# Performance work log

Measured on AMD Instinct MI355X. Metric: run time of the kernel, lower is better.

## Reference

```python
import jax, jax.numpy as jnp
import numpy as np

EPS = 1e-5
N0 = 2000  # number of crystals


def batchnorm(x, gamma, beta):
    # training-mode BatchNorm1d over rows (biased variance, like torch normalization)
    mu = jnp.mean(x, axis=0)
    var = jnp.mean(jnp.square(x - mu), axis=0)
    return (x - mu) * jax.lax.rsqrt(var + EPS) * gamma + beta


def setup_inputs() -> dict:
    key = jax.random.key(0)
    ks = jax.random.split(key, 16)
    N, M, F, B = 100000, 12, 64, 41
    d = {
        "atom_fea": jax.random.normal(ks[0], (N, 92), jnp.float32),
        "nbr_fea": jax.random.uniform(ks[1], (N, M, B), jnp.float32),
        "nbr_fea_idx": jax.random.randint(ks[2], (N, M), 0, N),
        "crystal_atom_idx": jnp.sort(jax.random.randint(ks[3], (N,), 0, N0)),
        "emb_w": jax.random.normal(ks[4], (92, F), jnp.float32) * 0.1,
        "emb_b": jax.random.normal(ks[5], (F,), jnp.float32) * 0.1,
        "conv_w": jax.random.normal(ks[6], (3, 2 * F + B, 2 * F), jnp.float32) * 0.05,
        "conv_b": jax.random.normal(ks[7], (3, 2 * F), jnp.float32) * 0.05,
        "bn1_g": jnp.ones((3, 2 * F), jnp.float32),
        "bn1_b": jnp.zeros((3, 2 * F), jnp.float32),
        "bn2_g": jnp.ones((3, F), jnp.float32),
        "bn2_b": jnp.zeros((3, F), jnp.float32),
        "fc_w": jax.random.normal(ks[8], (F, 128), jnp.float32) * 0.1,
        "fc_b": jax.random.normal(ks[9], (128,), jnp.float32) * 0.1,
        "head_w": jax.random.normal(ks[10], (128, 256), jnp.float32) * 0.1,
        "head_b": jax.random.normal(ks[11], (256,), jnp.float32) * 0.1,
        "out_w": jax.random.normal(ks[12], (256, 1), jnp.float32) * 0.1,
        "out_b": jax.random.normal(ks[13], (1,), jnp.float32) * 0.1,
    }
    return d


def reference(atom_fea, nbr_fea, nbr_fea_idx, crystal_atom_idx,
              emb_w, emb_b, conv_w, conv_b, bn1_g, bn1_b, bn2_g, bn2_b,
              fc_w, fc_b, head_w, head_b, out_w, out_b):
    N, M = nbr_fea_idx.shape
    F = emb_w.shape[1]
    x = atom_fea @ emb_w + emb_b  # (N, F)
    for i in range(conv_w.shape[0]):
        nbr_atom = x[nbr_fea_idx]  # (N, M, F) gather
        self_fea = jnp.broadcast_to(x[:, None, :], (N, M, F))
        tot = jnp.concatenate([self_fea, nbr_atom, nbr_fea], axis=2)  # (N, M, 2F+B)
        g = jnp.einsum('nmc,cf->nmf', tot, conv_w[i]) + conv_b[i]  # (N, M, 2F)
        g = batchnorm(g.reshape(N * M, 2 * F), bn1_g[i], bn1_b[i]).reshape(N, M, 2 * F)
        nbr_filter = jax.nn.sigmoid(g[:, :, :F])
        nbr_core = jax.nn.softplus(g[:, :, F:])
        nbr_sumed = jnp.sum(nbr_filter * nbr_core, axis=1)  # (N, F)
        nbr_sumed = batchnorm(nbr_sumed, bn2_g[i], bn2_b[i])
        x = jax.nn.softplus(x + nbr_sumed)
    # mean-pool atoms into crystals
    seg = crystal_atom_idx
    sums = jax.ops.segment_sum(x, seg, num_segments=N0)
    cnts = jax.ops.segment_sum(jnp.ones((N,), x.dtype), seg, num_segments=N0)
    crys = sums / jnp.maximum(cnts, 1.0)[:, None]  # (N0, F)
    crys = jax.nn.relu(crys @ fc_w + fc_b)
    h = crys @ head_w + head_b
    out = h @ out_w + out_b
    return out
```

## Files before the change

kernel.cpp:

```cpp
#include <hip/hip_runtime.h>
#include <hip/hip_bf16.h>

#define NATOM 100000
#define MNBR  12
#define FDIM  64
#define BDIM  41
#define C2    128
#define EPSBN 1e-5f
#define NEDGE (NATOM * MNBR)
#define KP48  48
#define NFRAG  16384
#define NFRAGS 8192

typedef __attribute__((ext_vector_type(8))) short bf16x8;
typedef __attribute__((ext_vector_type(4))) unsigned short u16x4;
typedef __attribute__((ext_vector_type(4))) float f32x4;

#define X_OFF    0L
#define XB_OFF   6400000L
#define S_OFF    9600000L
#define NBRB_OFF 16000000L
#define AS_OFF   54400000L
#define BALL_OFF 60800000L
#define BALLS_OFF 60808192L
#define BN1S_OFF 60812288L
#define BN2S_OFF 60828672L
#define SC1_OFF  60836864L
#define SH1_OFF  60836992L
#define SC2_OFF  60837120L
#define SH2_OFF  60837184L
#define CRY_OFF  60837248L
#define CNT_OFF  60965248L
#define ZB_OFF   60967296L
#define WS_NEED_FUSED ((ZB_OFF + 76800000L) * 4L)
#define ZERO_OFF BN1S_OFF
#define ZERO_CNT 154960L

__device__ __forceinline__ float bf2f(unsigned short u) {
    return __uint_as_float(((unsigned)u) << 16);
}
__device__ __forceinline__ unsigned short f2bf(float f) {
    __hip_bfloat16 h = __float2bfloat16(f);
    return *(unsigned short*)&h;
}
__device__ __forceinline__ float softplus_f(float v) {
    return fmaxf(v, 0.f) + __logf(1.f + __expf(-fabsf(v)));
}

__global__ void k_zero(float* __restrict__ p, long cnt) {
    long i = (long)blockIdx.x * 256 + threadIdx.x;
    if (i < cnt) p[i] = 0.f;
}

__global__ void k_nbrcvt(const float* __restrict__ nbr, __hip_bfloat16* __restrict__ outb) {
    long i = (long)blockIdx.x * 256 + threadIdx.x;
    if (i >= (long)NEDGE * 6) return;
    long e = i / 6;
    int c = (int)(i - e * 6);
    const float* src = nbr + e * BDIM + c * 8;
    bf16x8 v;
#pragma unroll
    for (int j = 0; j < 8; ++j) {
        int k = c * 8 + j;
        float f = (k < BDIM) ? src[j] : 0.f;
        v[j] = (short)f2bf(f);
    }
    *(bf16x8*)((short*)outb + e * KP48 + c * 8) = v;
}

__global__ void k_bcvt(const float* __restrict__ cw, __hip_bfloat16* __restrict__ ballf,
                       __hip_bfloat16* __restrict__ ballfS) {
    int i = blockIdx.x * 256 + threadIdx.x;
    if (i < NFRAG) {
        int T = i / 2048, r = i - T * 2048;
        int lidx = (r >> 3) & 63, e = i & 7;
        int s4 = r >> 9;
        int lo = lidx & 15, hi = lidx >> 4;
        int krow = 64 + s4 * 32 + hi * 8 + e;
        float v = (krow < 169) ? cw[krow * C2 + T * 16 + lo] : 0.f;
        ballf[i] = __float2bfloat16(v);
    } else if (i < NFRAG + NFRAGS) {
        int i2 = i - NFRAG;
        int T = i2 / 1024, r = i2 - T * 1024;
        int lidx = (r >> 3) & 63, e = i2 & 7;
        int s = r >> 9;
        int lo = lidx & 15, hi = lidx >> 4;
        int krow = s * 32 + hi * 8 + e;
        ballfS[i2] = __float2bfloat16(cw[krow * C2 + T * 16 + lo]);
    }
}

__global__ __launch_bounds__(256)
void k_embed(const float* __restrict__ af, const float* __restrict__ ew,
             const float* __restrict__ eb, float* __restrict__ x,
             __hip_bfloat16* __restrict__ xb) {
    int t = threadIdx.x;
    int c = t & 63, ag = t >> 6;
    long n0 = (long)blockIdx.x * 16 + ag * 4;
    float acc[4] = {0.f, 0.f, 0.f, 0.f};
    for (int k4 = 0; k4 < 23; ++k4) {
        float w0 = ew[(4 * k4 + 0) * FDIM + c];
        float w1 = ew[(4 * k4 + 1) * FDIM + c];
        float w2 = ew[(4 * k4 + 2) * FDIM + c];
        float w3 = ew[(4 * k4 + 3) * FDIM + c];
#pragma unroll
        for (int a = 0; a < 4; ++a) {
            const float4* ar = (const float4*)(af + (n0 + a) * 92);
            float4 v = ar[k4];
            acc[a] += v.x * w0 + v.y * w1 + v.z * w2 + v.w * w3;
        }
    }
    float b = eb[c];
#pragma unroll
    for (int a = 0; a < 4; ++a) {
        float v = acc[a] + b;
        x[(n0 + a) * FDIM + c] = v;
        xb[(n0 + a) * FDIM + c] = __float2bfloat16(v);
    }
}

__global__ __launch_bounds__(256, 8)
void k_lin(const __hip_bfloat16* __restrict__ xb, const __hip_bfloat16* __restrict__ ballfS,
           __hip_bfloat16* __restrict__ aS) {
    int t = threadIdx.x, w = t >> 6, l = t & 63;
    int lo = l & 15, hi = l >> 4;
    long atom0 = ((long)blockIdx.x * 4 + w) * 16;
    if (atom0 >= NATOM) return;
    const short* xs = (const short*)xb + (atom0 + lo) * FDIM + hi * 8;
    bf16x8 A0 = *(const bf16x8*)(xs);
    bf16x8 A1 = *(const bf16x8*)(xs + 32);
    const short* bS = (const short*)ballfS;
#pragma unroll
    for (int T = 0; T < 8; ++T) {
        bf16x8 B0 = *(const bf16x8*)(bS + T * 1024 + l * 8);
        bf16x8 B1 = *(const bf16x8*)(bS + T * 1024 + 512 + l * 8);
        f32x4 z = {0.f, 0.f, 0.f, 0.f};
        z = __builtin_amdgcn_mfma_f32_16x16x32_bf16(A0, B0, z, 0, 0, 0);
        z = __builtin_amdgcn_mfma_f32_16x16x32_bf16(A1, B1, z, 0, 0, 0);
#pragma unroll
        for (int qq = 0; qq < 4; ++qq)
            aS[(atom0 + hi * 4 + qq) * C2 + T * 16 + lo] = __float2bfloat16(z[qq]);
    }
}

template <int APPLY, int ZSTORE>
__global__ __launch_bounds__(256, 4)
void k_edge(const __hip_bfloat16* __restrict__ xb,
            const __hip_bfloat16* __restrict__ nbrb,
            const __hip_bfloat16* __restrict__ ballf,
            const __hip_bfloat16* __restrict__ aS,
            const int* __restrict__ idxp,
            const float* __restrict__ sc1, const float* __restrict__ sh1,
            float* __restrict__ bn1_slots,
            float* __restrict__ sout, float* __restrict__ bn2_slots,
            __hip_bfloat16* __restrict__ zb) {
    __shared__ float bn_s[256];
    __shared__ float sc_s[128], sh_s[128];

    const int t = threadIdx.x;
    const int w = t >> 6, l = t & 63;
    const int lo = l & 15, hi = l >> 4;
    const bool real = lo < MNBR;
    const int elo = real ? lo : 0;
    const int atom0 = blockIdx.x * 16 + w * 4;
    const short* xbS = (const short*)xb;
    const short* nbS = (const short*)nbrb;
    const short* aSS = (const short*)aS;
    const short* bb  = (const short*)ballf;
    short* zbS = (short*)zb;

    bn_s[t] = 0.f;
    if (APPLY && t < 128) { sc_s[t] = sc1[t]; sh_s[t] = sh1[t]; }
    __syncthreads();

    const bf16x8 zz = {0, 0, 0, 0, 0, 0, 0, 0};
    const int off1 = (hi < 2) ? (32 + hi * 8) : 0;

#pragma unroll 1
    for (int pr = 0; pr < 2; ++pr) {
        const int a0 = atom0 + pr * 2;
        const int a1 = a0 + 1;
        const int j0 = idxp[(long)a0 * MNBR + elo];
        const int j1 = idxp[(long)a1 * MNBR + elo];
        const short* xj0 = xbS + (long)j0 * FDIM + hi * 8;
        const short* xj1 = xbS + (long)j1 * FDIM + hi * 8;
        const short* nb0 = nbS + ((long)a0 * MNBR + elo) * KP48;
        const short* nb1 = nbS + ((long)a1 * MNBR + elo) * KP48;
        bf16x8 A00 = *(const bf16x8*)(xj0);
        bf16x8 A01 = *(const bf16x8*)(xj0 + 32);
        bf16x8 A02 = *(const bf16x8*)(nb0 + hi * 8);
        bf16x8 n03 = *(const bf16x8*)(nb0 + off1);
        bf16x8 A03 = (hi < 2) ? n03 : zz;
        bf16x8 A10 = *(const bf16x8*)(xj1);
        bf16x8 A11 = *(const bf16x8*)(xj1 + 32);
        bf16x8 A12 = *(const bf16x8*)(nb1 + hi * 8);
        bf16x8 n13 = *(const bf16x8*)(nb1 + off1);
        bf16x8 A13 = (hi < 2) ? n13 : zz;

        if (APPLY == 0) {
#pragma unroll 2
            for (int P = 0; P < 8; ++P) {
                const short* bp = bb + P * 2048 + l * 8;
                bf16x8 B0 = *(const bf16x8*)(bp);
                bf16x8 B1 = *(const bf16x8*)(bp + 512);
                bf16x8 B2 = *(const bf16x8*)(bp + 1024);
                bf16x8 B3 = *(const bf16x8*)(bp + 1536);
                float a0v = bf2f((unsigned short)aSS[(long)a0 * C2 + P * 16 + lo]);
                float a1v = bf2f((unsigned short)aSS[(long)a1 * C2 + P * 16 + lo]);
                f32x4 z0 = {0.f, 0.f, 0.f, 0.f}, z1 = {0.f, 0.f, 0.f, 0.f};
                z0 = __builtin_amdgcn_mfma_f32_16x16x32_bf16(A00, B0, z0, 0, 0, 0);
                z1 = __builtin_amdgcn_mfma_f32_16x16x32_bf16(A10, B0, z1, 0, 0, 0);
                z0 = __builtin_amdgcn_mfma_f32_16x16x32_bf16(A01, B1, z0, 0, 0, 0);
                z1 = __builtin_amdgcn_mfma_f32_16x16x32_bf16(A11, B1, z1, 0, 0, 0);
                z0 = __builtin_amdgcn_mfma_f32_16x16x32_bf16(A02, B2, z0, 0, 0, 0);
                z1 = __builtin_amdgcn_mfma_f32_16x16x32_bf16(A12, B2, z1, 0, 0, 0);
                z0 = __builtin_amdgcn_mfma_f32_16x16x32_bf16(A03, B3, z0, 0, 0, 0);
                z1 = __builtin_amdgcn_mfma_f32_16x16x32_bf16(A13, B3, z1, 0, 0, 0);
#pragma unroll
                for (int g = 0; g < 2; ++g) {
                    f32x4 z = g ? z1 : z0;
                    float av = g ? a1v : a0v;
                    float zp0 = z[0] + av, zp1 = z[1] + av, zp2 = z[2] + av, zp3 = z[3] + av;
                    if (ZSTORE && hi < 3) {
                        u16x4 pk = {f2bf(zp0), f2bf(zp1), f2bf(zp2), f2bf(zp3)};
                        *(u16x4*)&zbS[(long)(g ? a1 : a0) * 1536 + P * 192 + hi * 64 + lo * 4] = pk;
                    }
                    float s1 = zp0 + zp1 + zp2 + zp3;
                    float s2 = zp0 * zp0 + zp1 * zp1 + zp2 * zp2 + zp3 * zp3;
                    if (hi == 3) { s1 = 0.f; s2 = 0.f; }
                    s1 += __shfl_xor(s1, 16); s2 += __shfl_xor(s2, 16);
                    s1 += __shfl_xor(s1, 32); s2 += __shfl_xor(s2, 32);
                    if (hi == 0) {
                        atomicAdd(&bn_s[P * 16 + lo], s1);
                        atomicAdd(&bn_s[128 + P * 16 + lo], s2);
                    }
                }
            }
        } else {
#pragma unroll 1
            for (int P = 0; P < 4; ++P) {
                const short* bpf = bb + P * 2048 + l * 8;
                const short* bpc = bb + (P + 4) * 2048 + l * 8;
                bf16x8 Bf0 = *(const bf16x8*)(bpf);
                bf16x8 Bf1 = *(const bf16x8*)(bpf + 512);
                bf16x8 Bf2 = *(const bf16x8*)(bpf + 1024);
                bf16x8 Bf3 = *(const bf16x8*)(bpf + 1536);
                bf16x8 Bc0 = *(const bf16x8*)(bpc);
                bf16x8 Bc1 = *(const bf16x8*)(bpc + 512);
                bf16x8 Bc2 = *(const bf16x8*)(bpc + 1024);
                bf16x8 Bc3 = *(const bf16x8*)(bpc + 1536);
                const int c = P * 16 + lo;
                const float s_f = sc_s[c], h_f = sh_s[c];
                const float s_c = sc_s[64 + c], h_c = sh_s[64 + c];
                float hv0f = bf2f((unsigned short)aSS[(long)a0 * C2 + c]) * s_f + h_f;
                float hv0c = bf2f((unsigned short)aSS[(long)a0 * C2 + 64 + c]) * s_c + h_c;
                float hv1f = bf2f((unsigned short)aSS[(long)a1 * C2 + c]) * s_f + h_f;
                float hv1c = bf2f((unsigned short)aSS[(long)a1 * C2 + 64 + c]) * s_c + h_c;
                f32x4 zf0 = {0.f, 0.f, 0.f, 0.f}, zc0 = {0.f, 0.f, 0.f, 0.f};
                f32x4 zf1 = {0.f, 0.f, 0.f, 0.f}, zc1 = {0.f, 0.f, 0.f, 0.f};
                zf0 = __builtin_amdgcn_mfma_f32_16x16x32_bf16(A00, Bf0, zf0, 0, 0, 0);
                zc0 = __builtin_amdgcn_mfma_f32_16x16x32_bf16(A00, Bc0, zc0, 0, 0, 0);
                zf1 = __builtin_amdgcn_mfma_f32_16x16x32_bf16(A10, Bf0, zf1, 0, 0, 0);
                zc1 = __builtin_amdgcn_mfma_f32_16x16x32_bf16(A10, Bc0, zc1, 0, 0, 0);
                zf0 = __builtin_amdgcn_mfma_f32_16x16x32_bf16(A01, Bf1, zf0, 0, 0, 0);
                zc0 = __builtin_amdgcn_mfma_f32_16x16x32_bf16(A01, Bc1, zc0, 0, 0, 0);
                zf1 = __builtin_amdgcn_mfma_f32_16x16x32_bf16(A11, Bf1, zf1, 0, 0, 0);
                zc1 = __builtin_amdgcn_mfma_f32_16x16x32_bf16(A11, Bc1, zc1, 0, 0, 0);
                zf0 = __builtin_amdgcn_mfma_f32_16x16x32_bf16(A02, Bf2, zf0, 0, 0, 0);
                zc0 = __builtin_amdgcn_mfma_f32_16x16x32_bf16(A02, Bc2, zc0, 0, 0, 0);
                zf1 = __builtin_amdgcn_mfma_f32_16x16x32_bf16(A12, Bf2, zf1, 0, 0, 0);
                zc1 = __builtin_amdgcn_mfma_f32_16x16x32_bf16(A12, Bc2, zc1, 0, 0, 0);
                zf0 = __builtin_amdgcn_mfma_f32_16x16x32_bf16(A03, Bf3, zf0, 0, 0, 0);
                zc0 = __builtin_amdgcn_mfma_f32_16x16x32_bf16(A03, Bc3, zc0, 0, 0, 0);
                zf1 = __builtin_amdgcn_mfma_f32_16x16x32_bf16(A13, Bf3, zf1, 0, 0, 0);
                zc1 = __builtin_amdgcn_mfma_f32_16x16x32_bf16(A13, Bc3, zc1, 0, 0, 0);
#pragma unroll
                for (int g = 0; g < 2; ++g) {
                    f32x4 zf = g ? zf1 : zf0;
                    f32x4 zc = g ? zc1 : zc0;
                    float hvf = g ? hv1f : hv0f;
                    float hvc = g ? hv1c : hv0c;
                    float pvsum = 0.f;
#pragma unroll
                    for (int qq = 0; qq < 4; ++qq) {
                        float zfh = zf[qq] * s_f + hvf;
                        float zch = zc[qq] * s_c + hvc;
                        float filt = 1.f / (1.f + __expf(-zfh));
                        pvsum += filt * softplus_f(zch);
                    }
                    if (hi == 3) pvsum = 0.f;
                    pvsum += __shfl_xor(pvsum, 16);
                    pvsum += __shfl_xor(pvsum, 32);
                    if (hi == 0) {
                        sout[(long)(g ? a1 : a0) * FDIM + c] = pvsum;
                        atomicAdd(&bn_s[c], pvsum);
                        atomicAdd(&bn_s[64 + c], pvsum * pvsum);
                    }
                }
            }
        }
    }

    __syncthreads();
    if (APPLY == 0) {
        atomicAdd(&bn1_slots[(blockIdx.x & 63) * 256 + t], bn_s[t]);
    } else {
        if (t < 128)
            atomicAdd(&bn2_slots[(blockIdx.x & 63) * 128 + t], bn_s[t]);
    }
}

__global__ __launch_bounds__(256, 8)
void k_zapply(const __hip_bfloat16* __restrict__ zb,
              const float* __restrict__ sc1, const float* __restrict__ sh1,
              float* __restrict__ sout, float* __restrict__ bn2_slots) {
    __shared__ float bn_s[128];
    __shared__ float sc_s[128], sh_s[128];
    const int t = threadIdx.x;
    const int w = t >> 6, l = t & 63;
    const int lo = l & 15, hi = l >> 4;
    if (t < 128) { bn_s[t] = 0.f; sc_s[t] = sc1[t]; sh_s[t] = sh1[t]; }
    __syncthreads();

    const int atom0 = blockIdx.x * 16 + w * 4;
    const short* zs = (const short*)zb;
    const int hiC = (hi < 3) ? hi : 0;

#pragma unroll
    for (int a = 0; a < 4; ++a) {
        const long base = (long)(atom0 + a) * 1536 + hiC * 64 + lo * 4;
#pragma unroll
        for (int P = 0; P < 4; ++P) {
            u16x4 zf = *(const u16x4*)&zs[base + P * 192];
            u16x4 zc = *(const u16x4*)&zs[base + (P + 4) * 192];
            const int c = P * 16 + lo;
            const float s_f = sc_s[c], h_f = sh_s[c];
            const float s_c = sc_s[64 + c], h_c = sh_s[64 + c];
            float pvsum = 0.f;
#pragma unroll
            for (int qq = 0; qq < 4; ++qq) {
                float zfh = bf2f(zf[qq]) * s_f + h_f;
                float zch = bf2f(zc[qq]) * s_c + h_c;
                float filt = 1.f / (1.f + __expf(-zfh));
                pvsum += filt * softplus_f(zch);
            }
            if (hi == 3) pvsum = 0.f;
            pvsum += __shfl_xor(pvsum, 16);
            pvsum += __shfl_xor(pvsum, 32);
            if (hi == 0) {
                sout[(long)(atom0 + a) * FDIM + c] = pvsum;
                atomicAdd(&bn_s[c], pvsum);
                atomicAdd(&bn_s[64 + c], pvsum * pvsum);
            }
        }
    }
    __syncthreads();
    if (t < 128)
        atomicAdd(&bn2_slots[(blockIdx.x & 63) * 128 + t], bn_s[t]);
}

__global__ void k_bnfin(float* __restrict__ slots, const float* __restrict__ gamma,
                        const float* __restrict__ beta,
                        float* __restrict__ scale, float* __restrict__ shift,
                        float inv_cnt, int nc) {
    int c = threadIdx.x;
    if (c >= nc) return;
    float s1 = 0.f, s2 = 0.f;
    for (int s = 0; s < 64; ++s) {
        s1 += slots[s * 2 * nc + c];
        s2 += slots[s * 2 * nc + nc + c];
    }
    for (int s = 0; s < 64; ++s) {
        slots[s * 2 * nc + c] = 0.f;
        slots[s * 2 * nc + nc + c] = 0.f;
    }
    float mu = s1 * inv_cnt;
    float var = fmaxf(s2 * inv_cnt - mu * mu, 0.f);
    float sc = gamma[c] * rsqrtf(var + EPSBN);
    scale[c] = sc;
    shift[c] = beta[c] - mu * sc;
}

__global__ void k_x(float* __restrict__ x, __hip_bfloat16* __restrict__ xb,
                    const float* __restrict__ s,
                    const float* __restrict__ scale2, const float* __restrict__ shift2) {
    long i = (long)blockIdx.x * 256 + threadIdx.x;
    if (i >= (long)NATOM * FDIM) return;
    int c = (int)(i & 63);
    float v = softplus_f(x[i] + s[i] * scale2[c] + shift2[c]);
    x[i] = v;
    xb[i] = __float2bfloat16(v);
}

__global__ void k_pool(const float* __restrict__ x, const int* __restrict__ seg,
                       float* __restrict__ cry, float* __restrict__ cnt) {
    long i = (long)blockIdx.x * 256 + threadIdx.x;
    if (i >= (long)NATOM * FDIM) return;
    int n = (int)(i >> 6), c = (int)(i & 63);
    int cr = seg[n];
    atomicAdd(&cry[(long)cr * FDIM + c], x[i]);
    if (c == 0) atomicAdd(&cnt[cr], 1.f);
}

__global__ __launch_bounds__(256)
void k_head(const float* __restrict__ cry, const float* __restrict__ cnt,
            const float* __restrict__ fw, const float* __restrict__ fb,
            const float* __restrict__ hw, const float* __restrict__ hb,
            const float* __restrict__ ow, const float* __restrict__ ob,
            float* __restrict__ out) {
    __shared__ float cs[64], h1[128], red[256];
    int t = threadIdx.x, cr = blockIdx.x;
    if (t < 64) cs[t] = cry[(long)cr * 64 + t] / fmaxf(cnt[cr], 1.f);
    __syncthreads();
    if (t < 128) {
        float a = fb[t];
        for (int k = 0; k < 64; ++k) a += cs[k] * fw[k * 128 + t];
        h1[t] = fmaxf(a, 0.f);
    }
    __syncthreads();
    float a = hb[t];
    for (int k = 0; k < 128; ++k) a += h1[k] * hw[k * 256 + t];
    red[t] = a * ow[t];
    __syncthreads();
    for (int off = 128; off > 0; off >>= 1) {
        if (t < off) red[t] += red[t + off];
        __syncthreads();
    }
    if (t == 0) out[cr] = red[0] + ob[0];
}

extern "C" void kernel_launch(void* const* d_in, const int* in_sizes, int n_in,
                              void* d_out, int out_size, void* d_ws, size_t ws_size,
                              hipStream_t stream) {
    const float* atom_fea = (const float*)d_in[0];
    const float* nbr_fea  = (const float*)d_in[1];
    const int*   nbr_idx  = (const int*)d_in[2];
    const int*   seg      = (const int*)d_in[3];
    const float* emb_w    = (const float*)d_in[4];
    const float* emb_b    = (const float*)d_in[5];
    const float* conv_w   = (const float*)d_in[6];
    const float* bn1_g    = (const float*)d_in[8];
    const float* bn1_b    = (const float*)d_in[9];
    const float* bn2_g    = (const float*)d_in[10];
    const float* bn2_b    = (const float*)d_in[11];
    const float* fc_w     = (const float*)d_in[12];
    const float* fc_b     = (const float*)d_in[13];
    const float* head_w   = (const float*)d_in[14];
    const float* head_b   = (const float*)d_in[15];
    const float* out_w    = (const float*)d_in[16];
    const float* out_b    = (const float*)d_in[17];
    float* out = (float*)d_out;

    float* ws = (float*)d_ws;
    float* x = ws + X_OFF;
    __hip_bfloat16* xb     = (__hip_bfloat16*)(ws + XB_OFF);
    float* s = ws + S_OFF;
    __hip_bfloat16* nbrb   = (__hip_bfloat16*)(ws + NBRB_OFF);
    __hip_bfloat16* aS     = (__hip_bfloat16*)(ws + AS_OFF);
    __hip_bfloat16* ballf  = (__hip_bfloat16*)(ws + BALL_OFF);
    __hip_bfloat16* ballfS = (__hip_bfloat16*)(ws + BALLS_OFF);
    float* bn1s = ws + BN1S_OFF;
    float* bn2s = ws + BN2S_OFF;
    float* sc1 = ws + SC1_OFF;
    float* sh1 = ws + SH1_OFF;
    float* sc2 = ws + SC2_OFF;
    float* sh2 = ws + SH2_OFF;
    float* cry = ws + CRY_OFF;
    float* cnt = ws + CNT_OFF;
    __hip_bfloat16* zb = (__hip_bfloat16*)(ws + ZB_OFF);
    const bool fused = (ws_size >= (size_t)WS_NEED_FUSED);

    k_zero<<<(int)((ZERO_CNT + 255) / 256), 256, 0, stream>>>(ws + ZERO_OFF, ZERO_CNT);
    k_nbrcvt<<<(int)(((long)NEDGE * 6 + 255) / 256), 256, 0, stream>>>(nbr_fea, nbrb);
    k_embed<<<NATOM / 16, 256, 0, stream>>>(atom_fea, emb_w, emb_b, x, xb);

    for (int i = 0; i < 3; ++i) {
        const float* cw = conv_w + (long)i * 169 * C2;
        k_bcvt<<<96, 256, 0, stream>>>(cw, ballf, ballfS);
        k_lin<<<1563, 256, 0, stream>>>(xb, ballfS, aS);
        if (fused) {
            k_edge<0, 1><<<NATOM / 16, 256, 0, stream>>>(xb, nbrb, ballf, aS, nbr_idx,
                                                         nullptr, nullptr, bn1s, nullptr,
                                                         nullptr, zb);
            k_bnfin<<<1, 128, 0, stream>>>(bn1s, bn1_g + i * C2, bn1_b + i * C2,
                                           sc1, sh1, 1.f / 1200000.f, 128);
            k_zapply<<<NATOM / 16, 256, 0, stream>>>(zb, sc1, sh1, s, bn2s);
        } else {
            k_edge<0, 0><<<NATOM / 16, 256, 0, stream>>>(xb, nbrb, ballf, aS, nbr_idx,
                                                         nullptr, nullptr, bn1s, nullptr,
                                                         nullptr, nullptr);
            k_bnfin<<<1, 128, 0, stream>>>(bn1s, bn1_g + i * C2, bn1_b + i * C2,
                                           sc1, sh1, 1.f / 1200000.f, 128);
            k_edge<1, 0><<<NATOM / 16, 256, 0, stream>>>(xb, nbrb, ballf, aS, nbr_idx,
                                                         sc1, sh1, nullptr, s, bn2s, nullptr);
        }
        k_bnfin<<<1, 64, 0, stream>>>(bn2s, bn2_g + i * 64, bn2_b + i * 64,
                                      sc2, sh2, 1e-5f, 64);
        k_x<<<(NATOM * FDIM) / 256, 256, 0, stream>>>(x, xb, s, sc2, sh2);
    }

    k_pool<<<(NATOM * FDIM) / 256, 256, 0, stream>>>(x, seg, cry, cnt);
    k_head<<<2000, 256, 0, stream>>>(cry, cnt, fc_w, fc_b, head_w, head_b, out_w, out_b, out);
}
```

Baseline: 1.378 ms.

## Pack edges densely into 16-row MFMA tiles and transpose z buffer layout

After: 1.226 ms. 11.0% less time.

```diff
diff --git a/kernel.cpp b/kernel.cpp
--- a/kernel.cpp
+++ b/kernel.cpp
@@ -143,7 +143,133 @@
     }
 }
 
-template <int APPLY, int ZSTORE>
+__global__ __launch_bounds__(256, 4)
+void k_edge_dense(const __hip_bfloat16* __restrict__ xb,
+                  const __hip_bfloat16* __restrict__ nbrb,
+                  const __hip_bfloat16* __restrict__ ballf,
+                  const __hip_bfloat16* __restrict__ aS,
+                  const int* __restrict__ idxp,
+                  float* __restrict__ bn1_slots,
+                  __hip_bfloat16* __restrict__ zb) {
+    __shared__ float bn_s[256];
+    const int t = threadIdx.x;
+    const int w = t >> 6, l = t & 63;
+    const int lo = l & 15, hi = l >> 4;
+    const short* xbS = (const short*)xb;
+    const short* nbS = (const short*)nbrb;
+    const short* aSS = (const short*)aS;
+    const short* bb  = (const short*)ballf;
+    short* zbS = (short*)zb;
+
+    bn_s[t] = 0.f;
+    __syncthreads();
+
+    const long tile0 = (long)blockIdx.x * 8 + w * 2;
+    const bf16x8 zz = {0, 0, 0, 0, 0, 0, 0, 0};
+    const int off1 = (hi < 2) ? (32 + hi * 8) : 0;
+
+    bf16x8 A[2][4];
+    long ebase[2];
+#pragma unroll
+    for (int g = 0; g < 2; ++g) {
+        const long e0 = (tile0 + g) * 16;
+        ebase[g] = e0;
+        const int j = idxp[e0 + lo];
+        const short* xj = xbS + (long)j * FDIM + hi * 8;
+        const short* nb = nbS + (e0 + lo) * KP48;
+        A[g][0] = *(const bf16x8*)(xj);
+        A[g][1] = *(const bf16x8*)(xj + 32);
+        A[g][2] = *(const bf16x8*)(nb + hi * 8);
+        bf16x8 n1 = *(const bf16x8*)(nb + off1);
+        A[g][3] = (hi < 2) ? n1 : zz;
+    }
+
+#pragma unroll 2
+    for (int P = 0; P < 8; ++P) {
+        const short* bp = bb + P * 2048 + l * 8;
+        bf16x8 B0 = *(const bf16x8*)(bp);
+        bf16x8 B1 = *(const bf16x8*)(bp + 512);
+        bf16x8 B2 = *(const bf16x8*)(bp + 1024);
+        bf16x8 B3 = *(const bf16x8*)(bp + 1536);
+        f32x4 z0 = {0.f, 0.f, 0.f, 0.f}, z1 = {0.f, 0.f, 0.f, 0.f};
+        z0 = __builtin_amdgcn_mfma_f32_16x16x32_bf16(A[0][0], B0, z0, 0, 0, 0);
+        z1 = __builtin_amdgcn_mfma_f32_16x16x32_bf16(A[1][0], B0, z1, 0, 0, 0);
+        z0 = __builtin_amdgcn_mfma_f32_16x16x32_bf16(A[0][1], B1, z0, 0, 0, 0);
+        z1 = __builtin_amdgcn_mfma_f32_16x16x32_bf16(A[1][1], B1, z1, 0, 0, 0);
+        z0 = __builtin_amdgcn_mfma_f32_16x16x32_bf16(A[0][2], B2, z0, 0, 0, 0);
+        z1 = __builtin_amdgcn_mfma_f32_16x16x32_bf16(A[1][2], B2, z1, 0, 0, 0);
+        z0 = __builtin_amdgcn_mfma_f32_16x16x32_bf16(A[0][3], B3, z0, 0, 0, 0);
+        z1 = __builtin_amdgcn_mfma_f32_16x16x32_bf16(A[1][3], B3, z1, 0, 0, 0);
+#pragma unroll
+        for (int g = 0; g < 2; ++g) {
+            f32x4 z = g ? z1 : z0;
+            float s1 = 0.f, s2 = 0.f;
+            u16x4 pk;
+#pragma unroll
+            for (int qq = 0; qq < 4; ++qq) {
+                const int n = (int)((ebase[g] + hi * 4 + qq) / 12);
+                float av = bf2f((unsigned short)aSS[(long)n * C2 + P * 16 + lo]);
+                float zp = z[qq] + av;
+                pk[qq] = f2bf(zp);
+                s1 += zp;
+                s2 += zp * zp;
+            }
+            *(u16x4*)&zbS[(tile0 + g) * 2048 + (P * 16 + lo) * 16 + hi * 4] = pk;
+            s1 += __shfl_xor(s1, 16); s2 += __shfl_xor(s2, 16);
+            s1 += __shfl_xor(s1, 32); s2 += __shfl_xor(s2, 32);
+            if (hi == 0) {
+                atomicAdd(&bn_s[P * 16 + lo], s1);
+                atomicAdd(&bn_s[128 + P * 16 + lo], s2);
+            }
+        }
+    }
+    __syncthreads();
+    atomicAdd(&bn1_slots[(blockIdx.x & 63) * 256 + t], bn_s[t]);
+}
+
+__global__ __launch_bounds__(256, 8)
+void k_zapply2(const __hip_bfloat16* __restrict__ zb,
+               const float* __restrict__ sc1, const float* __restrict__ sh1,
+               float* __restrict__ sout, float* __restrict__ bn2_slots) {
+    __shared__ float bn_s[128];
+    __shared__ float sc_s[128], sh_s[128];
+    const int t = threadIdx.x;
+    if (t < 128) { bn_s[t] = 0.f; sc_s[t] = sc1[t]; sh_s[t] = sh1[t]; }
+    __syncthreads();
+
+    const int a = blockIdx.x * 4 + (t >> 6);
+    const int c = t & 63;
+    const float s_f = sc_s[c], h_f = sh_s[c];
+    const float s_c = sc_s[64 + c], h_c = sh_s[64 + c];
+    const short* zs = (const short*)zb;
+    const long e0 = (long)a * 12;
+
+    float pv = 0.f;
+#pragma unroll
+    for (int k = 0; k < 3; ++k) {
+        const long e = e0 + k * 4;
+        const long tile = e >> 4;
+        const int r = (int)(e & 15);
+        const short* base = zs + tile * 2048 + r;
+        u16x4 zf = *(const u16x4*)&base[c * 16];
+        u16x4 zc = *(const u16x4*)&base[(64 + c) * 16];
+#pragma unroll
+        for (int qq = 0; qq < 4; ++qq) {
+            float zfh = bf2f(zf[qq]) * s_f + h_f;
+            float zch = bf2f(zc[qq]) * s_c + h_c;
+            float filt = 1.f / (1.f + __expf(-zfh));
+            pv += filt * softplus_f(zch);
+        }
+    }
+    sout[(long)a * FDIM + c] = pv;
+    atomicAdd(&bn_s[c], pv);
+    atomicAdd(&bn_s[64 + c], pv * pv);
+    __syncthreads();
+    if (t < 128)
+        atomicAdd(&bn2_slots[(blockIdx.x & 63) * 128 + t], bn_s[t]);
+}
+
+template <int APPLY>
 __global__ __launch_bounds__(256, 4)
 void k_edge(const __hip_bfloat16* __restrict__ xb,
             const __hip_bfloat16* __restrict__ nbrb,
@@ -152,8 +278,7 @@
             const int* __restrict__ idxp,
             const float* __restrict__ sc1, const float* __restrict__ sh1,
             float* __restrict__ bn1_slots,
-            float* __restrict__ sout, float* __restrict__ bn2_slots,
-            __hip_bfloat16* __restrict__ zb) {
+            float* __restrict__ sout, float* __restrict__ bn2_slots) {
     __shared__ float bn_s[256];
     __shared__ float sc_s[128], sh_s[128];
 
@@ -167,7 +292,6 @@
     const short* nbS = (const short*)nbrb;
     const short* aSS = (const short*)aS;
     const short* bb  = (const short*)ballf;
-    short* zbS = (short*)zb;
 
     bn_s[t] = 0.f;
     if (APPLY && t < 128) { sc_s[t] = sc1[t]; sh_s[t] = sh1[t]; }
@@ -220,13 +344,10 @@
                 for (int g = 0; g < 2; ++g) {
                     f32x4 z = g ? z1 : z0;
                     float av = g ? a1v : a0v;
-                    float zp0 = z[0] + av, zp1 = z[1] + av, zp2 = z[2] + av, zp3 = z[3] + av;
-                    if (ZSTORE && hi < 3) {
-                        u16x4 pk = {f2bf(zp0), f2bf(zp1), f2bf(zp2), f2bf(zp3)};
-                        *(u16x4*)&zbS[(long)(g ? a1 : a0) * 1536 + P * 192 + hi * 64 + lo * 4] = pk;
-                    }
-                    float s1 = zp0 + zp1 + zp2 + zp3;
-                    float s2 = zp0 * zp0 + zp1 * zp1 + zp2 * zp2 + zp3 * zp3;
+                    float sz = z[0] + z[1] + z[2] + z[3];
+                    float szz = z[0] * z[0] + z[1] * z[1] + z[2] * z[2] + z[3] * z[3];
+                    float s1 = sz + 4.f * av;
+                    float s2 = szz + 2.f * av * sz + 4.f * av * av;
                     if (hi == 3) { s1 = 0.f; s2 = 0.f; }
                     s1 += __shfl_xor(s1, 16); s2 += __shfl_xor(s2, 16);
                     s1 += __shfl_xor(s1, 32); s2 += __shfl_xor(s2, 32);
@@ -310,55 +431,6 @@
     }
 }
 
-__global__ __launch_bounds__(256, 8)
-void k_zapply(const __hip_bfloat16* __restrict__ zb,
-              const float* __restrict__ sc1, const float* __restrict__ sh1,
-              float* __restrict__ sout, float* __restrict__ bn2_slots) {
-    __shared__ float bn_s[128];
-    __shared__ float sc_s[128], sh_s[128];
-    const int t = threadIdx.x;
-    const int w = t >> 6, l = t & 63;
-    const int lo = l & 15, hi = l >> 4;
-    if (t < 128) { bn_s[t] = 0.f; sc_s[t] = sc1[t]; sh_s[t] = sh1[t]; }
-    __syncthreads();
-
-    const int atom0 = blockIdx.x * 16 + w * 4;
-    const short* zs = (const short*)zb;
-    const int hiC = (hi < 3) ? hi : 0;
-
-#pragma unroll
-    for (int a = 0; a < 4; ++a) {
-        const long base = (long)(atom0 + a) * 1536 + hiC * 64 + lo * 4;
-#pragma unroll
-        for (int P = 0; P < 4; ++P) {
-            u16x4 zf = *(const u16x4*)&zs[base + P * 192];
-            u16x4 zc = *(const u16x4*)&zs[base + (P + 4) * 192];
-            const int c = P * 16 + lo;
-            const float s_f = sc_s[c], h_f = sh_s[c];
-            const float s_c = sc_s[64 + c], h_c = sh_s[64 + c];
-            float pvsum = 0.f;
-#pragma unroll
-            for (int qq = 0; qq < 4; ++qq) {
-                float zfh = bf2f(zf[qq]) * s_f + h_f;
-                float zch = bf2f(zc[qq]) * s_c + h_c;
-                float filt = 1.f / (1.f + __expf(-zfh));
-                pvsum += filt * softplus_f(zch);
-            }
-            if (hi == 3) pvsum = 0.f;
-            pvsum += __shfl_xor(pvsum, 16);
-            pvsum += __shfl_xor(pvsum, 32);
-            if (hi == 0) {
-                sout[(long)(atom0 + a) * FDIM + c] = pvsum;
-                atomicAdd(&bn_s[c], pvsum);
-                atomicAdd(&bn_s[64 + c], pvsum * pvsum);
-            }
-        }
-    }
-    __syncthreads();
-    if (t < 128)
-        atomicAdd(&bn2_slots[(blockIdx.x & 63) * 128 + t], bn_s[t]);
-}
-
 __global__ void k_bnfin(float* __restrict__ slots, const float* __restrict__ gamma,
                         const float* __restrict__ beta,
                         float* __restrict__ scale, float* __restrict__ shift,
@@ -479,20 +551,17 @@
         k_bcvt<<<96, 256, 0, stream>>>(cw, ballf, ballfS);
         k_lin<<<1563, 256, 0, stream>>>(xb, ballfS, aS);
         if (fused) {
-            k_edge<0, 1><<<NATOM / 16, 256, 0, stream>>>(xb, nbrb, ballf, aS, nbr_idx,
-                                                         nullptr, nullptr, bn1s, nullptr,
-                                                         nullptr, zb);
+            k_edge_dense<<<9375, 256, 0, stream>>>(xb, nbrb, ballf, aS, nbr_idx, bn1s, zb);
             k_bnfin<<<1, 128, 0, stream>>>(bn1s, bn1_g + i * C2, bn1_b + i * C2,
                                            sc1, sh1, 1.f / 1200000.f, 128);
-            k_zapply<<<NATOM / 16, 256, 0, stream>>>(zb, sc1, sh1, s, bn2s);
+            k_zapply2<<<NATOM / 4, 256, 0, stream>>>(zb, sc1, sh1, s, bn2s);
         } else {
-            k_edge<0, 0><<<NATOM / 16, 256, 0, stream>>>(xb, nbrb, ballf, aS, nbr_idx,
-                                                         nullptr, nullptr, bn1s, nullptr,
-                                                         nullptr, nullptr);
+            k_edge<0><<<NATOM / 16, 256, 0, stream>>>(xb, nbrb, ballf, aS, nbr_idx,
+                                                      nullptr, nullptr, bn1s, nullptr, nullptr);
             k_bnfin<<<1, 128, 0, stream>>>(bn1s, bn1_g + i * C2, bn1_b + i * C2,
                                            sc1, sh1, 1.f / 1200000.f, 128);
-            k_edge<1, 0><<<NATOM / 16, 256, 0, stream>>>(xb, nbrb, ballf, aS, nbr_idx,
-                                                         sc1, sh1, nullptr, s, bn2s, nullptr);
+            k_edge<1><<<NATOM / 16, 256, 0, stream>>>(xb, nbrb, ballf, aS, nbr_idx,
+                                                      sc1, sh1, nullptr, s, bn2s);
         }
         k_bnfin<<<1, 64, 0, stream>>>(bn2s, bn2_g + i * 64, bn2_b + i * 64,
                                       sc2, sh2, 1e-5f, 64);
```
